# Optimization experiments

Hardware: AMD Instinct MI355X
Metric: run time of the kernel (lower is better)

## Reference

```python
import jax, jax.numpy as jnp
import numpy as np

B, H1, W1 = 2, 64, 64
H2, W2 = 64, 64
DIM = 64    # query_latent_dim
CLD = 128   # cost_latent_dim
K = 8       # latent tokens in cost memory
HEADS = 8
CH = 1      # cost_heads_num
R = 4


def layer_norm(x, g, b, eps=1e-5):
    m = x.mean(-1, keepdims=True)
    v = ((x - m) ** 2).mean(-1, keepdims=True)
    return (x - m) / jnp.sqrt(v + eps) * g + b


def lin_pos_emb(x, dim):
    # LinearPositionEmbeddingSine: x [N,1,2] -> [N,1,dim]
    freq = jnp.linspace(0.0, dim // 4 - 1, dim // 4)
    a = 3.14 * x[..., 0:1] * freq / 200.0
    b = 3.14 * x[..., 1:2] * freq / 200.0
    return jnp.concatenate([jnp.sin(a), jnp.cos(a), jnp.sin(b), jnp.cos(b)], axis=-1)


def bilinear_sample(img, coords):
    # img: [N,C,H,W]; coords: [N,h,w,2] (x,y) pixel coords; zero padding, align_corners=True
    N, C, H, W = img.shape
    x, y = coords[..., 0], coords[..., 1]
    x0 = jnp.floor(x); y0 = jnp.floor(y)
    wx = x - x0; wy = y - y0
    nidx = jnp.arange(N)[:, None, None]

    def gather(xi, yi):
        valid = ((xi >= 0) & (xi <= W - 1) & (yi >= 0) & (yi <= H - 1)).astype(img.dtype)
        xc = jnp.clip(xi, 0, W - 1).astype(jnp.int32)
        yc = jnp.clip(yi, 0, H - 1).astype(jnp.int32)
        return img[nidx, :, yc, xc] * valid[..., None]  # [N,h,w,C]

    v00 = gather(x0, y0); v10 = gather(x0 + 1.0, y0)
    v01 = gather(x0, y0 + 1.0); v11 = gather(x0 + 1.0, y0 + 1.0)
    out = (v00 * ((1 - wx) * (1 - wy))[..., None] + v10 * (wx * (1 - wy))[..., None]
           + v01 * ((1 - wx) * wy)[..., None] + v11 * (wx * wy)[..., None])
    return out.transpose(0, 3, 1, 2)  # [N,C,h,w]


def encode_flow(cost_maps, coords1):
    b, _, h1, w1 = coords1.shape
    c = coords1.transpose(0, 2, 3, 1)  # [B,H1,W1,2]
    d = jnp.linspace(-float(R), float(R), 2 * R + 1)
    dy, dx = jnp.meshgrid(d, d, indexing='ij')
    delta = jnp.stack([dy, dx], axis=-1)  # [9,9,2]
    centroid = c.reshape(b * h1 * w1, 1, 1, 2)
    samp = centroid + delta[None]  # [B*H1*W1,9,9,2]
    corr = bilinear_sample(cost_maps, samp)  # [B*H1*W1,CH,9,9]
    return corr.reshape(b, h1, w1, -1).transpose(0, 3, 1, 2)  # [B,81*CH,H1,W1]


def upsample_flow(flow, mask):
    # convex upsample [H,W] -> [8H,8W]
    n, _, h, w = flow.shape
    m = jax.nn.softmax(mask.reshape(n, 1, 9, 8, 8, h, w), axis=2)
    f = jnp.pad(8.0 * flow, ((0, 0), (0, 0), (1, 1), (1, 1)))
    patches = jnp.stack([f[:, :, i:i + h, j:j + w] for i in range(3) for j in range(3)], axis=2)
    up = jnp.sum(m * patches[:, :, :, None, None], axis=2)  # [N,2,8,8,H,W]
    return up.transpose(0, 1, 4, 2, 5, 3).reshape(n, 2, 8 * h, 8 * w)


def setup_inputs() -> dict:
    key = jax.random.key(0)
    ks = jax.random.split(key, 16)
    Bn = B * H1 * W1
    ys, xs = np.meshgrid(np.arange(H1), np.arange(W1), indexing='ij')
    grid = jnp.asarray(np.stack([xs, ys], 0), jnp.float32)  # [2,H1,W1], (x,y)
    coords1 = jnp.broadcast_to(grid, (B, 2, H1, W1)) + 3.0 * jax.random.normal(ks[0], (B, 2, H1, W1), jnp.float32)
    s = 0.05
    return {
        'cost_maps': jax.random.normal(ks[1], (Bn, CH, H2, W2), jnp.float32),
        'cost_memory': jax.random.normal(ks[2], (Bn, K, CLD), jnp.float32),
        'coords1': coords1,
        'up_mask': jax.random.normal(ks[3], (B, 9 * 64, H1, W1), jnp.float32),
        'fte_w1': s * jax.random.normal(ks[4], (DIM, 81 * CH), jnp.float32),
        'fte_b1': jnp.zeros((DIM,), jnp.float32),
        'fte_w2': s * jax.random.normal(ks[5], (DIM, DIM), jnp.float32),
        'fte_b2': jnp.zeros((DIM,), jnp.float32),
        'ln1_g': jnp.ones((DIM,), jnp.float32),
        'ln1_b': jnp.zeros((DIM,), jnp.float32),
        'ln2_g': jnp.ones((DIM,), jnp.float32),
        'ln2_b': jnp.zeros((DIM,), jnp.float32),
        'wq': s * jax.random.normal(ks[6], (DIM, DIM), jnp.float32),
        'bq': jnp.zeros((DIM,), jnp.float32),
        'wk': s * jax.random.normal(ks[7], (CLD, DIM), jnp.float32),
        'bk': jnp.zeros((DIM,), jnp.float32),
        'wv': s * jax.random.normal(ks[8], (CLD, DIM), jnp.float32),
        'bv': jnp.zeros((DIM,), jnp.float32),
        'wp': s * jax.random.normal(ks[9], (2 * DIM, DIM), jnp.float32),
        'bp': jnp.zeros((DIM,), jnp.float32),
        'ffn_w1': s * jax.random.normal(ks[10], (DIM, DIM), jnp.float32),
        'ffn_b1': jnp.zeros((DIM,), jnp.float32),
        'ffn_w2': s * jax.random.normal(ks[11], (DIM, DIM), jnp.float32),
        'ffn_b2': jnp.zeros((DIM,), jnp.float32),
    }


def reference(cost_maps, cost_memory, coords1, up_mask,
              fte_w1, fte_b1, fte_w2, fte_b2,
              ln1_g, ln1_b, ln2_g, ln2_b,
              wq, bq, wk, bk, wv, bv, wp, bp,
              ffn_w1, ffn_b1, ffn_w2, ffn_b2):
    Bn = B * H1 * W1
    ys, xs = jnp.meshgrid(jnp.arange(H1, dtype=coords1.dtype), jnp.arange(W1, dtype=coords1.dtype), indexing='ij')
    coords0 = jnp.broadcast_to(jnp.stack([xs, ys], 0), (B, 2, H1, W1))

    # correlation-volume bilinear sampling (encode_flow_token)
    corr = encode_flow(cost_maps, coords1)  # [B,81*CH,H1,W1]

    # flow token encoder: 1x1 conv -> GELU -> 1x1 conv
    q = jnp.einsum('bchw,oc->bohw', corr, fte_w1) + fte_b1[None, :, None, None]
    q = jax.nn.gelu(q, approximate=False)
    q = jnp.einsum('bchw,oc->bohw', q, fte_w2) + fte_b2[None, :, None, None]
    query = q.transpose(0, 2, 3, 1).reshape(Bn, 1, DIM)

    # cross attention with linear sine position encoding of query coords
    qc = coords1.reshape(B, 2, H1 * W1).transpose(0, 2, 1).reshape(Bn, 1, 2)
    enc = lin_pos_emb(qc, DIM)
    short = query
    qn = layer_norm(query, ln1_g, ln1_b)
    qlin = (qn + enc) @ wq + bq            # [Bn,1,DIM]
    k = cost_memory @ wk + bk              # [Bn,K,DIM]
    v = cost_memory @ wv + bv
    hd = DIM // HEADS
    qh = qlin.reshape(Bn, 1, HEADS, hd).transpose(0, 2, 1, 3)
    kh = k.reshape(Bn, K, HEADS, hd).transpose(0, 2, 1, 3)
    vh = v.reshape(Bn, K, HEADS, hd).transpose(0, 2, 1, 3)
    attn = jax.nn.softmax(jnp.einsum('bhid,bhjd->bhij', qh, kh) * (hd ** -0.5), axis=-1)
    out = jnp.einsum('bhij,bhjd->bhid', attn, vh).transpose(0, 2, 1, 3).reshape(Bn, 1, DIM)
    x = jnp.concatenate([out, short], -1) @ wp + bp
    x = short + x
    xn = layer_norm(x, ln2_g, ln2_b)
    x = x + (jax.nn.gelu(xn @ ffn_w1 + ffn_b1, approximate=False) @ ffn_w2 + ffn_b2)
    cost_global = x.reshape(B, H1, W1, DIM).transpose(0, 3, 1, 2)

    # convex upsampling of the flow field
    flow_up = upsample_flow(coords1 - coords0, up_mask)  # [B,2,8*H1,8*W1]
    return (flow_up, cost_global)
```

## Files before the change

### kernel.cpp

```cpp
#include <hip/hip_runtime.h>
#include <math.h>

typedef _Float16 h2 __attribute__((ext_vector_type(2)));

#if __has_builtin(__builtin_amdgcn_fdot2)
#define FDOT2(a,b,c) __builtin_amdgcn_fdot2((a),(b),(c),false)
#else
__device__ __forceinline__ float FDOT2(h2 a, h2 b, float c){
    return c + (float)a.x*(float)b.x + (float)a.y*(float)b.y;
}
#endif

__device__ __forceinline__ h2 pk2(float x, float y){
#if __has_builtin(__builtin_amdgcn_cvt_pkrtz)
    return __builtin_bit_cast(h2, __builtin_amdgcn_cvt_pkrtz(x, y));
#else
    h2 r; r.x = (_Float16)x; r.y = (_Float16)y; return r;
#endif
}
__device__ __forceinline__ unsigned h2u(h2 v){ return __builtin_bit_cast(unsigned, v); }
__device__ __forceinline__ h2 uh2(unsigned v){ return __builtin_bit_cast(h2, v); }

__device__ __forceinline__ float dot8(uint4 w, uint4 v, float acc){
    acc = FDOT2(uh2(w.x), uh2(v.x), acc);
    acc = FDOT2(uh2(w.y), uh2(v.y), acc);
    acc = FDOT2(uh2(w.z), uh2(v.z), acc);
    acc = FDOT2(uh2(w.w), uh2(v.w), acc);
    return acc;
}

__device__ __forceinline__ float gelu_exact(float x){
    return 0.5f * x * (1.0f + erff(x * 0.70710678118654752f));
}
__device__ __forceinline__ float wave_sum64(float v){
    #pragma unroll
    for(int off = 32; off >= 1; off >>= 1) v += __shfl_xor(v, off, 64);
    return v;
}
__device__ __forceinline__ void lds_fence(){ __asm__ volatile("s_waitcnt lgkmcnt(0)" ::: "memory"); }

#define W1T_OFF 0
#define W2T_OFF 2816
#define WQ_OFF  5120
#define FW1_OFF 7424
#define FW2_OFF 9728
#define WV_OFF  12032
#define WP_OFF  16384
#define WK_OFF  20736
#define WTOT    25344

#define CMO   0
#define TUO   544
#define CORRO 1088
#define QPO   1132
#define CCO   1168
#define ASO   1232
#define PIXDW 1296
#define LDSDW (WTOT + 8*PIXDW)

__global__ void prep_weights(const float* __restrict__ w1, const float* __restrict__ w2,
                             const float* __restrict__ wq, const float* __restrict__ fw1,
                             const float* __restrict__ fw2, const float* __restrict__ wv,
                             const float* __restrict__ wp, const float* __restrict__ wk,
                             unsigned* __restrict__ ws){
    int idx = blockIdx.x * blockDim.x + threadIdx.x;
    if(idx >= WTOT) return;
    float a = 0.f, b = 0.f;
    if(idx < W2T_OFF){
        int t = idx / 44, cp = idx % 44;
        if(2*cp   < 81) a = w1[t*81 + 2*cp];
        if(2*cp+1 < 81) b = w1[t*81 + 2*cp+1];
    } else if(idx < WQ_OFF){
        int r = idx - W2T_OFF; int t = r / 36, cp = r % 36;
        if(cp < 32){ a = w2[t*64 + 2*cp]; b = w2[t*64 + 2*cp+1]; }
    } else if(idx < FW1_OFF){
        int r = idx - WQ_OFF; int t = r / 36, cp = r % 36;
        if(cp < 32){ a = wq[(2*cp)*64 + t]; b = wq[(2*cp+1)*64 + t]; }
    } else if(idx < FW2_OFF){
        int r = idx - FW1_OFF; int t = r / 36, cp = r % 36;
        if(cp < 32){ a = fw1[(2*cp)*64 + t]; b = fw1[(2*cp+1)*64 + t]; }
    } else if(idx < WV_OFF){
        int r = idx - FW2_OFF; int t = r / 36, cp = r % 36;
        if(cp < 32){ a = fw2[(2*cp)*64 + t]; b = fw2[(2*cp+1)*64 + t]; }
    } else if(idx < WP_OFF){
        int r = idx - WV_OFF; int t = r / 68, cp = r % 68;
        if(cp < 64){ a = wv[(2*cp)*64 + t]; b = wv[(2*cp+1)*64 + t]; }
    } else if(idx < WK_OFF){
        int r = idx - WP_OFF; int t = r / 68, cp = r % 68;
        if(cp < 64){ a = wp[(2*cp)*64 + t]; b = wp[(2*cp+1)*64 + t]; }
    } else {
        int r = idx - WK_OFF; int c = r / 36, hp = r % 36;
        if(hp < 32){ a = wk[c*64 + 2*hp]; b = wk[c*64 + 2*hp+1]; }
    }
    ws[idx] = h2u(pk2(a, b));
}

__device__ __forceinline__ float bilin(const float* __restrict__ cmap, float cx, float cy, int e){
    int i = e / 9, j = e - 9*i;
    float sx = cx + (float)(i - 4);
    float sy = cy + (float)(j - 4);
    float x0 = floorf(sx), y0 = floorf(sy);
    float wx = sx - x0,   wy = sy - y0;
    float acc = 0.f;
    #pragma unroll
    for(int dy = 0; dy < 2; dy++){
        #pragma unroll
        for(int dx = 0; dx < 2; dx++){
            float xf = x0 + (float)dx, yf = y0 + (float)dy;
            bool valid = (xf >= 0.f) && (xf <= 63.f) && (yf >= 0.f) && (yf <= 63.f);
            int xi = min(max((int)xf, 0), 63);
            int yi = min(max((int)yf, 0), 63);
            float v = valid ? cmap[yi*64 + xi] : 0.f;
            acc += v * ((dx ? wx : 1.f - wx) * (dy ? wy : 1.f - wy));
        }
    }
    return acc;
}

__global__ __launch_bounds__(512, 1) void decoder_main(
    const float* __restrict__ cost_maps, const float* __restrict__ cost_memory,
    const float* __restrict__ coords1, const unsigned* __restrict__ ws,
    const float* __restrict__ fte_b1, const float* __restrict__ fte_b2,
    const float* __restrict__ ln1_g, const float* __restrict__ ln1_b,
    const float* __restrict__ ln2_g, const float* __restrict__ ln2_b,
    const float* __restrict__ bq, const float* __restrict__ bv,
    const float* __restrict__ bp, const float* __restrict__ fb1,
    const float* __restrict__ fb2, float* __restrict__ out_cg)
{
    __shared__ unsigned sm[LDSDW];

    const int tid = threadIdx.x;
    const int wv  = tid >> 6;
    const int ln  = tid & 63;

    {
        const uint4* src = (const uint4*)ws;
        uint4* dst = (uint4*)sm;
        for(int i = tid; i < WTOT/4; i += 512) dst[i] = src[i];
    }
    const float b1v = fte_b1[ln], b2v = fte_b2[ln];
    const float g1v = ln1_g[ln], be1 = ln1_b[ln];
    const float g2v = ln2_g[ln], be2 = ln2_b[ln];
    const float bqv = bq[ln], bvv = bv[ln], bpv = bp[ln];
    const float f1v = fb1[ln], f2v = fb2[ln];
    __syncthreads();

    unsigned* P = sm + WTOT + wv * PIXDW;
    float*    Pf = (float*)P;

    const int h_ = ln & 7;
    const int c0 = ln >> 3;
    const int j_ = ln >> 3;
    const int h3 = ln >> 3;

    int pix = blockIdx.x * 32 + wv;
    const float4* cm4p = (const float4*)cost_memory;
    float4 cmv0 = cm4p[(size_t)pix*256 +   0 + ln];
    float4 cmv1 = cm4p[(size_t)pix*256 +  64 + ln];
    float4 cmv2 = cm4p[(size_t)pix*256 + 128 + ln];
    float4 cmv3 = cm4p[(size_t)pix*256 + 192 + ln];
    float cx = coords1[(pix >> 12)*8192 + (pix & 4095)];
    float cy = coords1[(pix >> 12)*8192 + 4096 + (pix & 4095)];

    #pragma unroll 1
    for(int g = 0; g < 4; g++){
        {
            float4 v; int l0, jt, cp0;
            #define STAGE(V, I4) \
                v = V; l0 = 4*((I4)*64 + ln); jt = l0 >> 7; cp0 = (l0 & 127) >> 1; \
                P[CMO + jt*68 + cp0]     = h2u(pk2(v.x, v.y)); \
                P[CMO + jt*68 + cp0 + 1] = h2u(pk2(v.z, v.w));
            STAGE(cmv0, 0) STAGE(cmv1, 1) STAGE(cmv2, 2) STAGE(cmv3, 3)
            #undef STAGE
        }
        {
            const float* cmap = cost_maps + (size_t)pix * 4096;
            float cv = bilin(cmap, cx, cy, ln);
            float pr = __shfl_xor(cv, 1, 64);
            if((ln & 1) == 0) P[CORRO + (ln >> 1)] = h2u(pk2(cv, pr));
            float c2 = 0.f;
            if(ln < 17) c2 = bilin(cmap, cx, cy, 64 + ln);
            float pr2 = __shfl_xor(c2, 1, 64);
            if(ln < 17 && (ln & 1) == 0){
                float bb = (ln == 16) ? 0.f : pr2;
                P[CORRO + 32 + (ln >> 1)] = h2u(pk2(c2, bb));
            }
            if(ln < 3) P[CORRO + 41 + ln] = 0u;
        }
        int npix = pix + 8;
        float4 n0, n1, n2, n3; float ncx = 0.f, ncy = 0.f;
        if(g < 3){
            n0 = cm4p[(size_t)npix*256 +   0 + ln];
            n1 = cm4p[(size_t)npix*256 +  64 + ln];
            n2 = cm4p[(size_t)npix*256 + 128 + ln];
            n3 = cm4p[(size_t)npix*256 + 192 + ln];
            ncx = coords1[(npix >> 12)*8192 + (npix & 4095)];
            ncy = coords1[(npix >> 12)*8192 + 4096 + (npix & 4095)];
        }
        lds_fence();

        float q1 = b1v;
        {
            const uint4* wr = (const uint4*)&sm[W1T_OFF + ln*44];
            const uint4* ar = (const uint4*)&P[CORRO];
            #pragma unroll
            for(int gg = 0; gg < 11; gg++) q1 = dot8(wr[gg], ar[gg], q1);
        }
        q1 = gelu_exact(q1);
        {
            float pr = __shfl_xor(q1, 1, 64);
            if((ln & 1) == 0) P[QPO + (ln >> 1)] = h2u(pk2(q1, pr));
        }
        lds_fence();
        float shortv = b2v;
        {
            const uint4* wr = (const uint4*)&sm[W2T_OFF + ln*36];
            const uint4* ar = (const uint4*)&P[QPO];
            #pragma unroll
            for(int gg = 0; gg < 8; gg++) shortv = dot8(wr[gg], ar[gg], shortv);
        }
        float mean = wave_sum64(shortv) * (1.f/64.f);
        float d0   = shortv - mean;
        float var  = wave_sum64(d0*d0) * (1.f/64.f);
        float qn   = d0 * rsqrtf(var + 1e-5f) * g1v + be1;
        {
            int   fi    = ln & 15;
            float coord = (ln < 32) ? cx : cy;
            float ang   = 3.14f * coord * (float)fi / 200.0f;
            float enc   = (ln & 16) ? cosf(ang) : sinf(ang);
            float qv    = qn + enc;
            float pr = __shfl_xor(qv, 1, 64);
            if((ln & 1) == 0) P[QPO + (ln >> 1)] = h2u(pk2(qv, pr));
        }
        lds_fence();
        float qlin = bqv;
        {
            const uint4* wr = (const uint4*)&sm[WQ_OFF + ln*36];
            const uint4* ar = (const uint4*)&P[QPO];
            #pragma unroll
            for(int gg = 0; gg < 8; gg++) qlin = dot8(wr[gg], ar[gg], qlin);
        }
        {
            uint4 qh4 = *(const uint4*)&P[QPO + h_*4];
            #pragma unroll
            for(int i = 0; i < 16; i++){
                int c = c0 + 8*i;
                uint4 wk4 = *(const uint4*)&sm[WK_OFF + c*36 + h_*4];
                float tv = dot8(wk4, qh4, 0.f);
                float prt = __shfl_xor(tv, 8, 64);
                if((c0 & 1) == 0) P[TUO + h_*68 + (c0 >> 1) + 4*i] = h2u(pk2(tv, prt));
            }
        }
        lds_fence();
        float sacc = 0.f;
        {
            const int hk = ln & 7;
            const uint4* cmr = (const uint4*)&P[CMO + j_*68];
            const uint4* tur = (const uint4*)&P[TUO + hk*68];
            #pragma unroll
            for(int gg = 0; gg < 16; gg++) sacc = dot8(cmr[gg], tur[gg], sacc);
        }
        float sc = sacc * 0.35355339059327373f;
        float mx = sc;
        mx = fmaxf(mx, __shfl_xor(mx,  8, 64));
        mx = fmaxf(mx, __shfl_xor(mx, 16, 64));
        mx = fmaxf(mx, __shfl_xor(mx, 32, 64));
        float ex = expf(sc - mx);
        float se = ex;
        se += __shfl_xor(se,  8, 64);
        se += __shfl_xor(se, 16, 64);
        se += __shfl_xor(se, 32, 64);
        Pf[ASO + ln] = ex / se;
        lds_fence();
        {
            h2 aj2[8];
            #pragma unroll
            for(int j = 0; j < 8; j++){
                float av = Pf[ASO + j*8 + h_];
                aj2[j] = pk2(av, av);
            }
            #pragma unroll
            for(int i = 0; i < 8; i++){
                int cp = c0 + 8*i;
                h2 u2 = pk2(0.f, 0.f);
                #pragma unroll
                for(int j = 0; j < 8; j++)
                    u2 += aj2[j] * uh2(P[CMO + j*68 + cp]);
                P[TUO + h_*68 + cp] = h2u(u2);
            }
        }
        lds_fence();
        float attno = bvv;
        {
            const uint4* ur = (const uint4*)&P[TUO + h3*68];
            const uint4* wr = (const uint4*)&sm[WV_OFF + ln*68];
            #pragma unroll
            for(int gg = 0; gg < 16; gg++) attno = dot8(ur[gg], wr[gg], attno);
        }
        {
            float pa = __shfl_xor(attno, 1, 64);
            if((ln & 1) == 0) P[CCO + (ln >> 1)] = h2u(pk2(attno, pa));
            float psv = __shfl_xor(shortv, 1, 64);
            if((ln & 1) == 0) P[CCO + 32 + (ln >> 1)] = h2u(pk2(shortv, psv));
        }
        lds_fence();
        float x = bpv;
        {
            const uint4* wr = (const uint4*)&sm[WP_OFF + ln*68];
            const uint4* ar = (const uint4*)&P[CCO];
            #pragma unroll
            for(int gg = 0; gg < 16; gg++) x = dot8(wr[gg], ar[gg], x);
        }
        x += shortv;
        float m2 = wave_sum64(x) * (1.f/64.f);
        float dd = x - m2;
        float v2 = wave_sum64(dd*dd) * (1.f/64.f);
        float xn = dd * rsqrtf(v2 + 1e-5f) * g2v + be2;
        {
            float pr = __shfl_xor(xn, 1, 64);
            if((ln & 1) == 0) P[QPO + (ln >> 1)] = h2u(pk2(xn, pr));
        }
        lds_fence();
        float h1v = f1v;
        {
            const uint4* wr = (const uint4*)&sm[FW1_OFF + ln*36];
            const uint4* ar = (const uint4*)&P[QPO];
            #pragma unroll
            for(int gg = 0; gg < 8; gg++) h1v = dot8(wr[gg], ar[gg], h1v);
        }
        h1v = gelu_exact(h1v);
        {
            float pr = __shfl_xor(h1v, 1, 64);
            if((ln & 1) == 0) P[QPO + (ln >> 1)] = h2u(pk2(h1v, pr));
        }
        lds_fence();
        float f2 = f2v;
        {
            const uint4* wr = (const uint4*)&sm[FW2_OFF + ln*36];
            const uint4* ar = (const uint4*)&P[QPO];
            #pragma unroll
            for(int gg = 0; gg < 8; gg++) f2 = dot8(wr[gg], ar[gg], f2);
        }
        x += f2;
        {
            int bb = pix >> 12, hh = (pix >> 6) & 63, ww = pix & 63;
            out_cg[(((size_t)(bb*64 + ln))*64 + hh)*64 + ww] = x;
        }
        pix = npix; cx = ncx; cy = ncy;
        cmv0 = n0; cmv1 = n1; cmv2 = n2; cmv3 = n3;
    }
}

__global__ __launch_bounds__(512) void upsample_kernel(
    const float* __restrict__ coords1, const float* __restrict__ up_mask,
    float* __restrict__ out)
{
    __shared__ float mtile[9 * 544];
    __shared__ float fxs[3 * 64];
    __shared__ float fys[3 * 64];

    const int r = blockIdx.x & 7;
    const int h = (blockIdx.x >> 3) & 63;
    const int b = blockIdx.x >> 9;
    const int id = threadIdx.x;

    {
        const int s_ = id >> 6, w_ = id & 63;
        #pragma unroll
        for(int k = 0; k < 9; k++){
            int c = k*64 + r*8 + s_;
            mtile[k*544 + s_*68 + w_] =
                up_mask[(((size_t)b*576 + c)*64 + h)*64 + w_];
        }
    }
    if(id < 192){
        const int i = id >> 6, w_ = id & 63;
        const int hh = h + i - 1;
        float fx = 0.f, fy = 0.f;
        if(hh >= 0 && hh < 64){
            fx = 8.f * (coords1[((b*2 + 0)*64 + hh)*64 + w_] - (float)w_);
            fy = 8.f * (coords1[((b*2 + 1)*64 + hh)*64 + w_] - (float)hh);
        }
        fxs[i*64 + w_] = fx;
        fys[i*64 + w_] = fy;
    }
    __syncthreads();

    const int w = id >> 3, s = id & 7;
    float m[9];
    #pragma unroll
    for(int k = 0; k < 9; k++) m[k] = mtile[k*544 + s*68 + w];
    float mx = m[0];
    #pragma unroll
    for(int k = 1; k < 9; k++) mx = fmaxf(mx, m[k]);
    float se = 0.f;
    #pragma unroll
    for(int k = 0; k < 9; k++){ m[k] = expf(m[k] - mx); se += m[k]; }
    float inv = 1.f / se;

    float ox = 0.f, oy = 0.f;
    #pragma unroll
    for(int k = 0; k < 9; k++){
        int i = k / 3, j = k % 3;
        int ww = w + j - 1;
        float fx = 0.f, fy = 0.f;
        if(ww >= 0 && ww < 64){
            fx = fxs[i*64 + ww];
            fy = fys[i*64 + ww];
        }
        ox += m[k] * fx;
        oy += m[k] * fy;
    }
    ox *= inv; oy *= inv;

    const size_t row = (size_t)(h*8 + r) * 512 + w*8 + s;
    out[(size_t)(b*2 + 0)*262144 + row] = ox;
    out[(size_t)(b*2 + 1)*262144 + row] = oy;
}

extern "C" void kernel_launch(void* const* d_in, const int* in_sizes, int n_in,
                              void* d_out, int out_size, void* d_ws, size_t ws_size,
                              hipStream_t stream)
{
    const float* cost_maps   = (const float*)d_in[0];
    const float* cost_memory = (const float*)d_in[1];
    const float* coords1     = (const float*)d_in[2];
    const float* up_mask     = (const float*)d_in[3];
    const float* fte_w1      = (const float*)d_in[4];
    const float* fte_b1      = (const float*)d_in[5];
    const float* fte_w2      = (const float*)d_in[6];
    const float* fte_b2      = (const float*)d_in[7];
    const float* ln1_g       = (const float*)d_in[8];
    const float* ln1_b       = (const float*)d_in[9];
    const float* ln2_g       = (const float*)d_in[10];
    const float* ln2_b       = (const float*)d_in[11];
    const float* wq          = (const float*)d_in[12];
    const float* bq          = (const float*)d_in[13];
    const float* wk          = (const float*)d_in[14];
    const float* bv          = (const float*)d_in[17];
    const float* wv          = (const float*)d_in[16];
    const float* wp          = (const float*)d_in[18];
    const float* bp          = (const float*)d_in[19];
    const float* fw1         = (const float*)d_in[20];
    const float* fb1         = (const float*)d_in[21];
    const float* fw2         = (const float*)d_in[22];
    const float* fb2         = (const float*)d_in[23];
    float* out = (float*)d_out;
    unsigned* wsu = (unsigned*)d_ws;

    prep_weights<<<(WTOT + 511)/512, 512, 0, stream>>>(
        fte_w1, fte_w2, wq, fw1, fw2, wv, wp, wk, wsu);

    decoder_main<<<256, 512, 0, stream>>>(cost_maps, cost_memory, coords1, wsu,
        fte_b1, fte_b2, ln1_g, ln1_b, ln2_g, ln2_b,
        bq, bv, bp, fb1, fb2,
        out + 2*2*512*512);

    upsample_kernel<<<2*64*8, 512, 0, stream>>>(coords1, up_mask, out);
}
```

Measured before the change: 271.3 us.

## Cache decoder weights in registers and halve waves per block

Each lane now loads its rows of several weight matrices (W2T, WQ, FW1, FW2, WV, WP, WK) from LDS into registers once, before the pixel loop, so the per-pixel matvecs read weights from registers. Blocks shrink from 8 to 4 waves, and each wave processes 8 pixels instead of 4, which keeps total coverage the same. Dot-product reductions are split into two independent accumulators to shorten dependency chains. The trade-off is very high VGPR pressure (about 88 uint4 per lane) and half the waves per block to hide latency, with possible register spills.

```diff
diff --git a/kernel.cpp b/kernel.cpp
--- a/kernel.cpp
+++ b/kernel.cpp
@@ -56,7 +56,8 @@
 #define CCO   1168
 #define ASO   1232
 #define PIXDW 1296
-#define LDSDW (WTOT + 8*PIXDW)
+#define NWAVE 4
+#define LDSDW (WTOT + NWAVE*PIXDW)
 
 __global__ void prep_weights(const float* __restrict__ w1, const float* __restrict__ w2,
                              const float* __restrict__ wq, const float* __restrict__ fw1,
@@ -117,7 +118,7 @@
     return acc;
 }
 
-__global__ __launch_bounds__(512, 1) void decoder_main(
+__global__ __launch_bounds__(256, 1) void decoder_main(
     const float* __restrict__ cost_maps, const float* __restrict__ cost_memory,
     const float* __restrict__ coords1, const unsigned* __restrict__ ws,
     const float* __restrict__ fte_b1, const float* __restrict__ fte_b2,
@@ -136,7 +137,7 @@
     {
         const uint4* src = (const uint4*)ws;
         uint4* dst = (uint4*)sm;
-        for(int i = tid; i < WTOT/4; i += 512) dst[i] = src[i];
+        for(int i = tid; i < WTOT/4; i += 256) dst[i] = src[i];
     }
     const float b1v = fte_b1[ln], b2v = fte_b2[ln];
     const float g1v = ln1_g[ln], be1 = ln1_b[ln];
@@ -145,13 +146,29 @@
     const float f1v = fb1[ln], f2v = fb2[ln];
     __syncthreads();
 
-    unsigned* P = sm + WTOT + wv * PIXDW;
-    float*    Pf = (float*)P;
-
     const int h_ = ln & 7;
     const int c0 = ln >> 3;
     const int j_ = ln >> 3;
     const int h3 = ln >> 3;
+
+    uint4 rW2T[8], rWQ[8], rFW1[8], rFW2[8], rWV[16], rWP[16], rWK[16];
+    #pragma unroll
+    for(int g = 0; g < 8; g++)  rW2T[g] = *(const uint4*)&sm[W2T_OFF + ln*36 + 4*g];
+    #pragma unroll
+    for(int g = 0; g < 8; g++)  rWQ[g]  = *(const uint4*)&sm[WQ_OFF  + ln*36 + 4*g];
+    #pragma unroll
+    for(int g = 0; g < 8; g++)  rFW1[g] = *(const uint4*)&sm[FW1_OFF + ln*36 + 4*g];
+    #pragma unroll
+    for(int g = 0; g < 8; g++)  rFW2[g] = *(const uint4*)&sm[FW2_OFF + ln*36 + 4*g];
+    #pragma unroll
+    for(int g = 0; g < 16; g++) rWV[g]  = *(const uint4*)&sm[WV_OFF  + ln*68 + 4*g];
+    #pragma unroll
+    for(int g = 0; g < 16; g++) rWP[g]  = *(const uint4*)&sm[WP_OFF  + ln*68 + 4*g];
+    #pragma unroll
+    for(int i = 0; i < 16; i++) rWK[i]  = *(const uint4*)&sm[WK_OFF + (c0 + 8*i)*36 + h_*4];
+
+    unsigned* P = sm + WTOT + wv * PIXDW;
+    float*    Pf = (float*)P;
 
     int pix = blockIdx.x * 32 + wv;
     const float4* cm4p = (const float4*)cost_memory;
@@ -163,7 +180,7 @@
     float cy = coords1[(pix >> 12)*8192 + 4096 + (pix & 4095)];
 
     #pragma unroll 1
-    for(int g = 0; g < 4; g++){
+    for(int g = 0; g < 8; g++){
         {
             float4 v; int l0, jt, cp0;
             #define STAGE(V, I4) \
@@ -187,9 +204,9 @@
             }
             if(ln < 3) P[CORRO + 41 + ln] = 0u;
         }
-        int npix = pix + 8;
+        int npix = pix + 4;
         float4 n0, n1, n2, n3; float ncx = 0.f, ncy = 0.f;
-        if(g < 3){
+        if(g < 7){
             n0 = cm4p[(size_t)npix*256 +   0 + ln];
             n1 = cm4p[(size_t)npix*256 +  64 + ln];
             n2 = cm4p[(size_t)npix*256 + 128 + ln];
@@ -199,26 +216,33 @@
         }
         lds_fence();
 
-        float q1 = b1v;
+        float q1a = b1v, q1b = 0.f;
         {
             const uint4* wr = (const uint4*)&sm[W1T_OFF + ln*44];
             const uint4* ar = (const uint4*)&P[CORRO];
             #pragma unroll
-            for(int gg = 0; gg < 11; gg++) q1 = dot8(wr[gg], ar[gg], q1);
-        }
-        q1 = gelu_exact(q1);
+            for(int gg = 0; gg < 10; gg += 2){
+                q1a = dot8(wr[gg],   ar[gg],   q1a);
+                q1b = dot8(wr[gg+1], ar[gg+1], q1b);
+            }
+            q1a = dot8(wr[10], ar[10], q1a);
+        }
+        float q1 = gelu_exact(q1a + q1b);
         {
             float pr = __shfl_xor(q1, 1, 64);
             if((ln & 1) == 0) P[QPO + (ln >> 1)] = h2u(pk2(q1, pr));
         }
         lds_fence();
-        float shortv = b2v;
-        {
-            const uint4* wr = (const uint4*)&sm[W2T_OFF + ln*36];
+        float sva = b2v, svb = 0.f;
+        {
             const uint4* ar = (const uint4*)&P[QPO];
             #pragma unroll
-            for(int gg = 0; gg < 8; gg++) shortv = dot8(wr[gg], ar[gg], shortv);
-        }
+            for(int gg = 0; gg < 8; gg += 2){
+                sva = dot8(rW2T[gg],   ar[gg],   sva);
+                svb = dot8(rW2T[gg+1], ar[gg+1], svb);
+            }
+        }
+        float shortv = sva + svb;
         float mean = wave_sum64(shortv) * (1.f/64.f);
         float d0   = shortv - mean;
         float var  = wave_sum64(d0*d0) * (1.f/64.f);
@@ -233,33 +257,38 @@
             if((ln & 1) == 0) P[QPO + (ln >> 1)] = h2u(pk2(qv, pr));
         }
         lds_fence();
-        float qlin = bqv;
-        {
-            const uint4* wr = (const uint4*)&sm[WQ_OFF + ln*36];
+        float qla = bqv, qlb = 0.f;
+        {
             const uint4* ar = (const uint4*)&P[QPO];
             #pragma unroll
-            for(int gg = 0; gg < 8; gg++) qlin = dot8(wr[gg], ar[gg], qlin);
-        }
+            for(int gg = 0; gg < 8; gg += 2){
+                qla = dot8(rWQ[gg],   ar[gg],   qla);
+                qlb = dot8(rWQ[gg+1], ar[gg+1], qlb);
+            }
+        }
+        float qlin = qla + qlb;
         {
             uint4 qh4 = *(const uint4*)&P[QPO + h_*4];
             #pragma unroll
             for(int i = 0; i < 16; i++){
-                int c = c0 + 8*i;
-                uint4 wk4 = *(const uint4*)&sm[WK_OFF + c*36 + h_*4];
-                float tv = dot8(wk4, qh4, 0.f);
+                float tv = dot8(rWK[i], qh4, 0.f);
                 float prt = __shfl_xor(tv, 8, 64);
                 if((c0 & 1) == 0) P[TUO + h_*68 + (c0 >> 1) + 4*i] = h2u(pk2(tv, prt));
             }
         }
         lds_fence();
-        float sacc = 0.f;
+        float sa = 0.f, sb = 0.f;
         {
             const int hk = ln & 7;
             const uint4* cmr = (const uint4*)&P[CMO + j_*68];
             const uint4* tur = (const uint4*)&P[TUO + hk*68];
             #pragma unroll
-            for(int gg = 0; gg < 16; gg++) sacc = dot8(cmr[gg], tur[gg], sacc);
-        }
+            for(int gg = 0; gg < 16; gg += 2){
+                sa = dot8(cmr[gg],   tur[gg],   sa);
+                sb = dot8(cmr[gg+1], tur[gg+1], sb);
+            }
+        }
+        float sacc = sa + sb;
         float sc = sacc * 0.35355339059327373f;
         float mx = sc;
         mx = fmaxf(mx, __shfl_xor(mx,  8, 64));
@@ -290,13 +319,16 @@
             }
         }
         lds_fence();
-        float attno = bvv;
+        float ata = bvv, atb = 0.f;
         {
             const uint4* ur = (const uint4*)&P[TUO + h3*68];
-            const uint4* wr = (const uint4*)&sm[WV_OFF + ln*68];
-            #pragma unroll
-            for(int gg = 0; gg < 16; gg++) attno = dot8(ur[gg], wr[gg], attno);
-        }
+            #pragma unroll
+            for(int gg = 0; gg < 16; gg += 2){
+                ata = dot8(ur[gg],   rWV[gg],   ata);
+                atb = dot8(ur[gg+1], rWV[gg+1], atb);
+            }
+        }
+        float attno = ata + atb;
         {
             float pa = __shfl_xor(attno, 1, 64);
             if((ln & 1) == 0) P[CCO + (ln >> 1)] = h2u(pk2(attno, pa));
@@ -304,14 +336,16 @@
             if((ln & 1) == 0) P[CCO + 32 + (ln >> 1)] = h2u(pk2(shortv, psv));
         }
         lds_fence();
-        float x = bpv;
-        {
-            const uint4* wr = (const uint4*)&sm[WP_OFF + ln*68];
+        float xa = bpv, xb = 0.f;
+        {
             const uint4* ar = (const uint4*)&P[CCO];
             #pragma unroll
-            for(int gg = 0; gg < 16; gg++) x = dot8(wr[gg], ar[gg], x);
-        }
-        x += shortv;
+            for(int gg = 0; gg < 16; gg += 2){
+                xa = dot8(rWP[gg],   ar[gg],   xa);
+                xb = dot8(rWP[gg+1], ar[gg+1], xb);
+            }
+        }
+        float x = xa + xb + shortv;
         float m2 = wave_sum64(x) * (1.f/64.f);
         float dd = x - m2;
         float v2 = wave_sum64(dd*dd) * (1.f/64.f);
@@ -321,27 +355,31 @@
             if((ln & 1) == 0) P[QPO + (ln >> 1)] = h2u(pk2(xn, pr));
         }
         lds_fence();
-        float h1v = f1v;
-        {
-            const uint4* wr = (const uint4*)&sm[FW1_OFF + ln*36];
+        float ha = f1v, hb = 0.f;
+        {
             const uint4* ar = (const uint4*)&P[QPO];
             #pragma unroll
-            for(int gg = 0; gg < 8; gg++) h1v = dot8(wr[gg], ar[gg], h1v);
-        }
-        h1v = gelu_exact(h1v);
+            for(int gg = 0; gg < 8; gg += 2){
+                ha = dot8(rFW1[gg],   ar[gg],   ha);
+                hb = dot8(rFW1[gg+1], ar[gg+1], hb);
+            }
+        }
+        float h1v = gelu_exact(ha + hb);
         {
             float pr = __shfl_xor(h1v, 1, 64);
             if((ln & 1) == 0) P[QPO + (ln >> 1)] = h2u(pk2(h1v, pr));
         }
         lds_fence();
-        float f2 = f2v;
-        {
-            const uint4* wr = (const uint4*)&sm[FW2_OFF + ln*36];
+        float fa = f2v, fb = 0.f;
+        {
             const uint4* ar = (const uint4*)&P[QPO];
             #pragma unroll
-            for(int gg = 0; gg < 8; gg++) f2 = dot8(wr[gg], ar[gg], f2);
-        }
-        x += f2;
+            for(int gg = 0; gg < 8; gg += 2){
+                fa = dot8(rFW2[gg],   ar[gg],   fa);
+                fb = dot8(rFW2[gg+1], ar[gg+1], fb);
+            }
+        }
+        x += fa + fb;
         {
             int bb = pix >> 12, hh = (pix >> 6) & 63, ww = pix & 63;
             out_cg[(((size_t)(bb*64 + ln))*64 + hh)*64 + ww] = x;
@@ -451,7 +489,7 @@
     prep_weights<<<(WTOT + 511)/512, 512, 0, stream>>>(
         fte_w1, fte_w2, wq, fw1, fw2, wv, wp, wk, wsu);
 
-    decoder_main<<<256, 512, 0, stream>>>(cost_maps, cost_memory, coords1, wsu,
+    decoder_main<<<256, 256, 0, stream>>>(cost_maps, cost_memory, coords1, wsu,
         fte_b1, fte_b2, ln1_g, ln1_b, ln2_g, ln2_b,
         bq, bv, bp, fb1, fb2,
         out + 2*2*512*512);
```

New measurement: 297.7 us. +9.7%, slower.
